# Optimization experiments

Measured on AMD Instinct MI355X. Metric: run time of the kernel, lower is better.

The kernel has to match this reference:

```python
import jax, jax.numpy as jnp
import numpy as np

B, D, K = 16384, 512, 8192
COMMITMENT_COST = 0.25


def setup_inputs() -> dict:
    key = jax.random.key(0)
    k1, k2 = jax.random.split(key)
    z = jax.random.normal(k1, (B, D), dtype=jnp.float32)
    embedding = jax.random.normal(k2, (K, D), dtype=jnp.float32)
    return {"z": z, "embedding": embedding}


def reference(z, embedding):
    # Squared L2 distances: ||z||^2 - 2 z E^T + ||e||^2  -> [B, K]
    distances = (
        jnp.sum(z * z, axis=-1, keepdims=True)
        - 2.0 * jnp.matmul(z, embedding.T)
        + jnp.sum(embedding * embedding, axis=-1)
    )
    indices = jnp.argmin(distances, axis=-1)  # [B]
    quantized = embedding[indices]  # [B, D] gather
    # use_ema=True branch: commitment loss only (codebook updated by EMA)
    commitment_loss = jnp.mean((z - jax.lax.stop_gradient(quantized)) ** 2)
    loss = COMMITMENT_COST * commitment_loss
    # Straight-through estimator
    quantized_st = z + jax.lax.stop_gradient(quantized - z)
    return quantized_st, indices, loss
```

## Files before the change

kernel.cpp:

```cpp
#include <hip/hip_runtime.h>
#include <hip/hip_bf16.h>

#define M_ROWS 16384
#define N_CODES 8192
#define DDIM    512
#define NCHUNK  512
#define MARGIN  4.0f

typedef unsigned int u32;
typedef unsigned long long u64;
typedef unsigned short u16;
typedef __attribute__((ext_vector_type(8))) short short8;
typedef __attribute__((ext_vector_type(4))) float f32x4;

__device__ __forceinline__ u32 float_to_ordered(float f) {
    u32 u = __float_as_uint(f);
    return (u & 0x80000000u) ? ~u : (u | 0x80000000u);
}

__device__ __forceinline__ u16 bf16_rne(float x) {
    u32 u = __float_as_uint(x);
    u32 r = u + 0x7FFFu + ((u >> 16) & 1u);
    return (u16)(r >> 16);
}

__device__ __forceinline__ void gl_lds16(const void* g, void* l) {
    __builtin_amdgcn_global_load_lds((const __attribute__((address_space(1))) u32*)g,
                                     (__attribute__((address_space(3))) u32*)l,
                                     16, 0, 0);
}

__device__ __forceinline__ u64 umin64(u64 a, u64 b) { return a < b ? a : b; }

#if __has_builtin(__builtin_amdgcn_update_dpp)
template <int CTRL>
__device__ __forceinline__ float dpp_mov(float x) {
    return __int_as_float(__builtin_amdgcn_update_dpp(
        __float_as_int(x), __float_as_int(x), CTRL, 0xF, 0xF, true));
}
#else
template <int CTRL>
__device__ __forceinline__ float dpp_mov(float x) {
    return __shfl_xor(x, CTRL == 0xB1 ? 1 : 2, 64);
}
#endif

__global__ __launch_bounds__(256) void vq_prep(
    const float4* __restrict__ z4, ushort4* __restrict__ zh,
    const float* __restrict__ emb, ushort4* __restrict__ eh,
    float* __restrict__ e_norms) {
    int b = blockIdx.x;
    if (b < (M_ROWS * DDIM) / 1024) {
        int i = b * 256 + threadIdx.x;
        float4 v = z4[i];
        ushort4 h;
        h.x = bf16_rne(v.x); h.y = bf16_rne(v.y);
        h.z = bf16_rne(v.z); h.w = bf16_rne(v.w);
        zh[i] = h;
    } else {
        int wave = threadIdx.x >> 6;
        int lane = threadIdx.x & 63;
        int code = (b - (M_ROWS * DDIM) / 1024) * 4 + wave;
        const float4* ep = (const float4*)(emb + (size_t)code * DDIM);
        size_t base4 = (size_t)code * (DDIM / 4);
        float s = 0.f;
        #pragma unroll
        for (int j = 0; j < 2; ++j) {
            int c = lane + 64 * j;
            float4 e = ep[c];
            s += e.x * e.x + e.y * e.y + e.z * e.z + e.w * e.w;
            ushort4 h;
            h.x = bf16_rne(e.x); h.y = bf16_rne(e.y);
            h.z = bf16_rne(e.z); h.w = bf16_rne(e.w);
            eh[base4 + c] = h;
        }
        #pragma unroll
        for (int off = 32; off; off >>= 1) s += __shfl_down(s, off, 64);
        if (lane == 0) e_norms[code] = s;
    }
}


__device__ __forceinline__ void stage_tile(const char* gbase, int kt,
                                           void* lds, int tid) {
    #pragma unroll
    for (int s = 0; s < 4; ++s) {
        const int row_l = (s << 6) + (tid >> 3);
        const int cb = (((tid & 7) ^ (row_l & 7)) << 4);
        const char* g = gbase + (size_t)row_l * (DDIM * 2) + ((size_t)kt << 7) + cb;
        char* l = (char*)lds + (s << 13) + (tid << 4);
        gl_lds16(g, l);
    }
}

#define BAR() __builtin_amdgcn_s_barrier()
#define LGK0() do { asm volatile("s_waitcnt lgkmcnt(0)" ::: "memory"); \
                    __builtin_amdgcn_sched_barrier(0); } while (0)
#define VMC8() do { asm volatile("s_waitcnt vmcnt(8)" ::: "memory"); } while (0)
#define VMC0() do { asm volatile("s_waitcnt vmcnt(0)" ::: "memory"); } while (0)

#define LDA(BUF, MH) do {                                                      \
    _Pragma("unroll") for (int i_ = 0; i_ < 4; ++i_) {                         \
        _Pragma("unroll") for (int kk_ = 0; kk_ < 2; ++kk_) {                  \
            const int row_ = (wm << 7) + ((((MH) << 2) + i_) << 4) + fr;       \
            const int cb_ = (kk_ << 6) + fkb;                                  \
            a[i_][kk_] = *(const short8*)((const char*)&ldsA[BUF][0][0]        \
                + row_ * 128 + (cb_ ^ ((row_ & 7) << 4)));                     \
        } } } while (0)

#define LDB(BUF, NH) do {                                                      \
    _Pragma("unroll") for (int j_ = 0; j_ < 2; ++j_) {                         \
        _Pragma("unroll") for (int kk_ = 0; kk_ < 2; ++kk_) {                  \
            const int row_ = (wn << 6) + ((((NH) << 1) + j_) << 4) + fr;       \
            const int cb_ = (kk_ << 6) + fkb;                                  \
            b[(NH) * 2 + j_][kk_] = *(const short8*)((const char*)&ldsB[BUF][0][0] \
                + row_ * 128 + (cb_ ^ ((row_ & 7) << 4)));                     \
        } } } while (0)

#define MFMA_Q(MH, NH) do {                                                    \
    __builtin_amdgcn_s_setprio(1);                                             \
    _Pragma("unroll") for (int i_ = 0; i_ < 4; ++i_) {                         \
        _Pragma("unroll") for (int j_ = 0; j_ < 2; ++j_) {                     \
            _Pragma("unroll") for (int kk_ = 0; kk_ < 2; ++kk_) {              \
                acc[(MH) * 4 + i_][(NH) * 2 + j_] =                            \
                    __builtin_amdgcn_mfma_f32_16x16x32_bf16(                   \
                        a[i_][kk_], b[(NH) * 2 + j_][kk_],                     \
                        acc[(MH) * 4 + i_][(NH) * 2 + j_], 0, 0, 0);           \
        } } }                                                                  \
    __builtin_amdgcn_s_setprio(0);                                             \
} while (0)

#define PH_ITER(SE, VMA, VMB, NK0, NK1)                                        \
    LDA(0, 0); LDB(0, 0);                                                      \
    BAR(); LGK0(); MFMA_Q(0, 0); BAR();                                        \
    LDB(0, 1);                                                                 \
    BAR(); LGK0(); MFMA_Q(0, 1); BAR();                                        \
    LDA(0, 1);                                                                 \
    if (SE) stage_tile(gB0, (NK0), &ldsB[0][0][0], tid);                       \
    BAR(); LGK0(); MFMA_Q(1, 0); BAR();                                        \
    if (SE) stage_tile(gA0, (NK0), &ldsA[0][0][0], tid);                       \
    BAR(); MFMA_Q(1, 1); VMA; BAR();                                           \
    LDA(1, 0); LDB(1, 0);                                                      \
    BAR(); LGK0(); MFMA_Q(0, 0); BAR();                                        \
    LDB(1, 1);                                                                 \
    BAR(); LGK0(); MFMA_Q(0, 1); BAR();                                        \
    LDA(1, 1);                                                                 \
    if (SE) stage_tile(gB0, (NK1), &ldsB[1][0][0], tid);                       \
    BAR(); LGK0(); MFMA_Q(1, 0); BAR();                                        \
    if (SE) stage_tile(gA0, (NK1), &ldsA[1][0][0], tid);                       \
    BAR(); MFMA_Q(1, 1); VMB; BAR();

__global__ __launch_bounds__(512, 2) void vq_phase1(
    const u16* __restrict__ z_hi, const u16* __restrict__ e_hi,
    const float* __restrict__ e_norms,
    float* __restrict__ chunkmin) {
    __shared__ __align__(16) u16 ldsA[2][256][64];
    __shared__ __align__(16) u16 ldsB[2][256][64];

    const int tid  = threadIdx.x;
    const int lane = tid & 63;
    const int wid  = tid >> 6;
    const int wm   = wid >> 2;
    const int wn   = wid & 3;
    const int row0 = blockIdx.x << 8;
    const int col0 = blockIdx.y << 8;
    const int fr   = lane & 15;
    const int fkb  = (lane >> 4) << 4;

    const char* gA0 = (const char*)z_hi + (size_t)row0 * (DDIM * 2);
    const char* gB0 = (const char*)e_hi + (size_t)col0 * (DDIM * 2);

    f32x4 acc[8][4] = {};
    short8 a[4][2], b[4][2];

    stage_tile(gA0, 0, &ldsA[0][0][0], tid);
    stage_tile(gB0, 0, &ldsB[0][0][0], tid);
    stage_tile(gA0, 1, &ldsA[1][0][0], tid);
    stage_tile(gB0, 1, &ldsB[1][0][0], tid);
    VMC8(); BAR();

    #pragma unroll 1
    for (int t = 0; t < 3; ++t) {
        const int nk0 = 2 * t + 2, nk1 = 2 * t + 3;
        PH_ITER(1, VMC8(), VMC8(), nk0, nk1)
    }
    PH_ITER(0, VMC0(), ((void)0), 0, 0)

    const int cn = lane & 15;
    const int cg = lane >> 4;
    float en[4];
    #pragma unroll
    for (int j = 0; j < 4; ++j) en[j] = e_norms[col0 + (wn << 6) + j * 16 + cn];

    #pragma unroll
    for (int i = 0; i < 8; ++i)
        #pragma unroll
        for (int r = 0; r < 4; ++r) {
            float mv[4];
            #pragma unroll
            for (int j = 0; j < 4; ++j) mv[j] = en[j] - 2.0f * acc[i][j][r];

            #pragma unroll
            for (int k = 0; k < 2; ++k) {
                float lo = mv[k], hi = mv[k + 2];
                float mine = (lane & 8) ? hi : lo;
                float thrs = (lane & 8) ? lo : hi;
                mv[k] = fminf(mine, __shfl_xor(thrs, 8, 64));
            }
            {
                float lo = mv[0], hi = mv[1];
                float mine = (lane & 4) ? hi : lo;
                float thrs = (lane & 4) ? lo : hi;
                mv[0] = fminf(mine, __shfl_xor(thrs, 4, 64));
            }
            mv[0] = fminf(mv[0], dpp_mov<0xB1>(mv[0]));
            mv[0] = fminf(mv[0], dpp_mov<0x4E>(mv[0]));

            if ((cn & 3) == 0) {
                const int jj = ((cn >> 3) << 1) | ((cn >> 2) & 1);
                const int row_g = row0 + (wm << 7) + (i << 4) + (cg << 2) + r;
                chunkmin[(size_t)row_g * NCHUNK + (col0 >> 4) + (wn << 2) + jj] = mv[0];
            }
        }
}

__global__ __launch_bounds__(256) void vq_finalize_rows(
    const float* __restrict__ z, const float* __restrict__ emb,
    const float* __restrict__ e_norms, const float* __restrict__ chunkmin,
    float* __restrict__ out_q, float* __restrict__ out_idx,
    float* __restrict__ partials) {
    const int wave = threadIdx.x >> 6;
    const int lane = threadIdx.x & 63;
    const int row  = blockIdx.x * 4 + wave;

    const float4* cm4 = (const float4*)(chunkmin + (size_t)row * NCHUNK);
    float4 v0 = cm4[lane];
    float4 v1 = cm4[64 + lane];
    float m = fminf(fminf(fminf(v0.x, v0.y), fminf(v0.z, v0.w)),
                    fminf(fminf(v1.x, v1.y), fminf(v1.z, v1.w)));
    #pragma unroll
    for (int off = 1; off < 64; off <<= 1) m = fminf(m, __shfl_xor(m, off, 64));
    const float thr = m + MARGIN;

    const float4* z4 = (const float4*)(z + (size_t)row * DDIM);
    float4 za = z4[2 * lane];
    float4 zb = z4[2 * lane + 1];

    u64 msk[8];
    msk[0] = __ballot(v0.x <= thr);
    msk[1] = __ballot(v0.y <= thr);
    msk[2] = __ballot(v0.z <= thr);
    msk[3] = __ballot(v0.w <= thr);
    msk[4] = __ballot(v1.x <= thr);
    msk[5] = __ballot(v1.y <= thr);
    msk[6] = __ballot(v1.z <= thr);
    msk[7] = __ballot(v1.w <= thr);

    const int cown = ((lane & 1) << 3) | ((lane & 2) << 1)
                   | ((lane & 4) >> 1) | ((lane & 8) >> 3);

    u64 best = 0xFFFFFFFFFFFFFFFFull;
    #pragma unroll
    for (int p = 0; p < 2; ++p)
        #pragma unroll
        for (int j = 0; j < 4; ++j) {
            u64 mk = msk[p * 4 + j];
            while (mk) {
                int l = __ffsll((long long)mk) - 1;
                mk &= mk - 1;
                const int chunk = (p << 8) + (l << 2) + j;
                const int cbase = chunk << 4;
                const float* eb = emb + (size_t)cbase * DDIM + lane * 8;
                float part[16];
                #pragma unroll
                for (int k = 0; k < 16; ++k) {
                    float4 ea = *(const float4*)(eb + (size_t)k * DDIM);
                    float4 e2 = *(const float4*)(eb + (size_t)k * DDIM + 4);
                    part[k] = za.x * ea.x + za.y * ea.y + za.z * ea.z + za.w * ea.w
                            + zb.x * e2.x + zb.y * e2.y + zb.z * e2.z + zb.w * e2.w;
                }
                #pragma unroll
                for (int k = 0; k < 8; ++k) {
                    float lo = part[k], hi = part[k + 8];
                    float mine = (lane & 1) ? hi : lo;
                    float thrs = (lane & 1) ? lo : hi;
                    part[k] = mine + dpp_mov<0xB1>(thrs);
                }
                #pragma unroll
                for (int k = 0; k < 4; ++k) {
                    float lo = part[k], hi = part[k + 4];
                    float mine = (lane & 2) ? hi : lo;
                    float thrs = (lane & 2) ? lo : hi;
                    part[k] = mine + dpp_mov<0x4E>(thrs);
                }
                #pragma unroll
                for (int k = 0; k < 2; ++k) {
                    float lo = part[k], hi = part[k + 2];
                    float mine = (lane & 4) ? hi : lo;
                    float thrs = (lane & 4) ? lo : hi;
                    part[k] = mine + __shfl_xor(thrs, 4, 64);
                }
                {
                    float lo = part[0], hi = part[1];
                    float mine = (lane & 8) ? hi : lo;
                    float thrs = (lane & 8) ? lo : hi;
                    part[0] = mine + __shfl_xor(thrs, 8, 64);
                }
                part[0] += __shfl_xor(part[0], 16, 64);
                part[0] += __shfl_xor(part[0], 32, 64);

                const int ci = cbase + cown;
                float dist = e_norms[ci] - 2.0f * part[0];
                best = umin64(best, ((u64)float_to_ordered(dist) << 32) | (u32)ci);
            }
        }

    #pragma unroll
    for (int off = 1; off < 64; off <<= 1)
        best = umin64(best, __shfl_xor(best, off, 64));

    const int idx = (int)(best & 0xFFFFFFFFull);
    const float* ew = emb + (size_t)idx * DDIM + lane * 8;
    float4 qa = *(const float4*)ew;
    float4 qb = *(const float4*)(ew + 4);
    float4* op = (float4*)(out_q + (size_t)row * DDIM);
    op[2 * lane]     = qa;
    op[2 * lane + 1] = qb;

    float dx, local = 0.f;
    dx = za.x - qa.x; local += dx * dx;  dx = za.y - qa.y; local += dx * dx;
    dx = za.z - qa.z; local += dx * dx;  dx = za.w - qa.w; local += dx * dx;
    dx = zb.x - qb.x; local += dx * dx;  dx = zb.y - qb.y; local += dx * dx;
    dx = zb.z - qb.z; local += dx * dx;  dx = zb.w - qb.w; local += dx * dx;
    #pragma unroll
    for (int off = 32; off; off >>= 1) local += __shfl_down(local, off, 64);

    __shared__ float wsum[4];
    if (lane == 0) { wsum[wave] = local; out_idx[row] = (float)idx; }
    __syncthreads();
    if (threadIdx.x == 0)
        partials[blockIdx.x] = wsum[0] + wsum[1] + wsum[2] + wsum[3];
}

__global__ __launch_bounds__(256) void vq_loss_reduce(
    const float* __restrict__ partials, float* __restrict__ out_loss) {
    __shared__ float red[256];
    float s = 0.f;
    for (int i = threadIdx.x; i < M_ROWS / 4; i += 256) s += partials[i];
    red[threadIdx.x] = s;
    __syncthreads();
    for (int off = 128; off; off >>= 1) {
        if (threadIdx.x < off) red[threadIdx.x] += red[threadIdx.x + off];
        __syncthreads();
    }
    if (threadIdx.x == 0)
        out_loss[0] = 0.25f * red[0] / ((float)M_ROWS * (float)DDIM);
}

extern "C" void kernel_launch(void* const* d_in, const int* in_sizes, int n_in,
                              void* d_out, int out_size, void* d_ws, size_t ws_size,
                              hipStream_t stream) {
    (void)in_sizes; (void)n_in; (void)out_size; (void)ws_size;
    const float* z   = (const float*)d_in[0];
    const float* emb = (const float*)d_in[1];

    float* out      = (float*)d_out;
    float* out_q    = out;
    float* out_idx  = out + (size_t)M_ROWS * DDIM;
    float* out_loss = out + (size_t)M_ROWS * DDIM + M_ROWS;

    char* ws = (char*)d_ws;
    float* e_norms  = (float*)ws;
    float* partials = (float*)(ws + 32768);
    u16* z_hi = (u16*)(ws + 49152);
    u16* e_hi = (u16*)(ws + 49152 + (size_t)M_ROWS * DDIM * 2);

    float* chunkmin = out_q;

    const int zblocks = (M_ROWS * DDIM) / 1024;
    const int eblocks = N_CODES / 4;
    vq_prep<<<zblocks + eblocks, 256, 0, stream>>>(
        (const float4*)z, (ushort4*)z_hi, emb, (ushort4*)e_hi, e_norms);

    vq_phase1<<<dim3(M_ROWS / 256, N_CODES / 256), 512, 0, stream>>>(
        z_hi, e_hi, e_norms, chunkmin);

    vq_finalize_rows<<<M_ROWS / 4, 256, 0, stream>>>(
        z, emb, e_norms, chunkmin, out_q, out_idx, partials);

    vq_loss_reduce<<<1, 256, 0, stream>>>(partials, out_loss);
}
```

Baseline: 356.8 us.

## Make phase1 GEMM persistent with eight row tiles per block and cross-tile prefetch

The phase-1 distance GEMM moves from a 64x32 grid of 256x256 tiles to 256 persistent blocks. Each block keeps one codebook column tile and walks 8 consecutive row tiles. The first k-slices of the next row tile are prefetched during the last k-iteration of the current one, which hides the per-tile pipeline fill and drain and keeps the codebook tile's norms in registers. In exchange, the grid of 256 blocks at two blocks per CU may leave some CUs idle or unbalanced on MI355X, and each tile's epilogue is now serialized inside the block.

```diff
diff --git a/kernel.cpp b/kernel.cpp
--- a/kernel.cpp
+++ b/kernel.cpp
@@ -98,6 +98,8 @@
                     __builtin_amdgcn_sched_barrier(0); } while (0)
 #define VMC8() do { asm volatile("s_waitcnt vmcnt(8)" ::: "memory"); } while (0)
 #define VMC0() do { asm volatile("s_waitcnt vmcnt(0)" ::: "memory"); } while (0)
+#define VMA_SEL() do { if (last) { VMC0(); } else { VMC8(); } } while (0)
+#define VMB_SEL() do { if (!last) { VMC8(); } } while (0)
 
 #define LDA(BUF, MH) do {                                                      \
     _Pragma("unroll") for (int i_ = 0; i_ < 4; ++i_) {                         \
@@ -130,24 +132,24 @@
     __builtin_amdgcn_s_setprio(0);                                             \
 } while (0)
 
-#define PH_ITER(SE, VMA, VMB, NK0, NK1)                                        \
+#define PH_ITER(SE, VMA, VMB, PA, PB, NK0, NK1)                                \
     LDA(0, 0); LDB(0, 0);                                                      \
     BAR(); LGK0(); MFMA_Q(0, 0); BAR();                                        \
     LDB(0, 1);                                                                 \
     BAR(); LGK0(); MFMA_Q(0, 1); BAR();                                        \
     LDA(0, 1);                                                                 \
-    if (SE) stage_tile(gB0, (NK0), &ldsB[0][0][0], tid);                       \
+    if (SE) stage_tile((PB), (NK0), &ldsB[0][0][0], tid);                      \
     BAR(); LGK0(); MFMA_Q(1, 0); BAR();                                        \
-    if (SE) stage_tile(gA0, (NK0), &ldsA[0][0][0], tid);                       \
+    if (SE) stage_tile((PA), (NK0), &ldsA[0][0][0], tid);                      \
     BAR(); MFMA_Q(1, 1); VMA; BAR();                                           \
     LDA(1, 0); LDB(1, 0);                                                      \
     BAR(); LGK0(); MFMA_Q(0, 0); BAR();                                        \
     LDB(1, 1);                                                                 \
     BAR(); LGK0(); MFMA_Q(0, 1); BAR();                                        \
     LDA(1, 1);                                                                 \
-    if (SE) stage_tile(gB0, (NK1), &ldsB[1][0][0], tid);                       \
+    if (SE) stage_tile((PB), (NK1), &ldsB[1][0][0], tid);                      \
     BAR(); LGK0(); MFMA_Q(1, 0); BAR();                                        \
-    if (SE) stage_tile(gA0, (NK1), &ldsA[1][0][0], tid);                       \
+    if (SE) stage_tile((PA), (NK1), &ldsA[1][0][0], tid);                      \
     BAR(); MFMA_Q(1, 1); VMB; BAR();
 
 __global__ __launch_bounds__(512, 2) void vq_phase1(
@@ -162,29 +164,18 @@
     const int wid  = tid >> 6;
     const int wm   = wid >> 2;
     const int wn   = wid & 3;
-    const int row0 = blockIdx.x << 8;
-    const int col0 = blockIdx.y << 8;
     const int fr   = lane & 15;
     const int fkb  = (lane >> 4) << 4;
 
-    const char* gA0 = (const char*)z_hi + (size_t)row0 * (DDIM * 2);
+    const int bcol  = blockIdx.x & 31;
+    const int brow0 = (blockIdx.x >> 5) << 3;
+    const int col0  = bcol << 8;
+
+    const char* gAb = (const char*)z_hi;
     const char* gB0 = (const char*)e_hi + (size_t)col0 * (DDIM * 2);
 
-    f32x4 acc[8][4] = {};
+    f32x4 acc[8][4];
     short8 a[4][2], b[4][2];
-
-    stage_tile(gA0, 0, &ldsA[0][0][0], tid);
-    stage_tile(gB0, 0, &ldsB[0][0][0], tid);
-    stage_tile(gA0, 1, &ldsA[1][0][0], tid);
-    stage_tile(gB0, 1, &ldsB[1][0][0], tid);
-    VMC8(); BAR();
-
-    #pragma unroll 1
-    for (int t = 0; t < 3; ++t) {
-        const int nk0 = 2 * t + 2, nk1 = 2 * t + 3;
-        PH_ITER(1, VMC8(), VMC8(), nk0, nk1)
-    }
-    PH_ITER(0, VMC0(), ((void)0), 0, 0)
 
     const int cn = lane & 15;
     const int cg = lane >> 4;
@@ -192,36 +183,64 @@
     #pragma unroll
     for (int j = 0; j < 4; ++j) en[j] = e_norms[col0 + (wn << 6) + j * 16 + cn];
 
-    #pragma unroll
-    for (int i = 0; i < 8; ++i)
+    {
+        const char* gA = gAb + ((size_t)brow0 << 8) * (DDIM * 2);
+        stage_tile(gA, 0, &ldsA[0][0][0], tid);
+        stage_tile(gB0, 0, &ldsB[0][0][0], tid);
+        stage_tile(gA, 1, &ldsA[1][0][0], tid);
+        stage_tile(gB0, 1, &ldsB[1][0][0], tid);
+    }
+    VMC8(); BAR();
+
+    #pragma unroll 1
+    for (int job = 0; job < 8; ++job) {
+        const int row0 = (brow0 + job) << 8;
+        const char* gAj = gAb + (size_t)row0 * (DDIM * 2);
+        const bool last = (job == 7);
+        const char* gAn = last ? gAj : (gAj + (size_t)256 * (DDIM * 2));
+
+        const f32x4 zf = {0.f, 0.f, 0.f, 0.f};
         #pragma unroll
-        for (int r = 0; r < 4; ++r) {
-            float mv[4];
+        for (int i = 0; i < 8; ++i)
             #pragma unroll
-            for (int j = 0; j < 4; ++j) mv[j] = en[j] - 2.0f * acc[i][j][r];
-
+            for (int j = 0; j < 4; ++j) acc[i][j] = zf;
+
+        PH_ITER(1, VMC8(), VMC8(), gAj, gB0, 2, 3)
+        PH_ITER(1, VMC8(), VMC8(), gAj, gB0, 4, 5)
+        PH_ITER(1, VMC8(), VMC8(), gAj, gB0, 6, 7)
+        PH_ITER(!last, VMA_SEL(), VMB_SEL(), gAn, gB0, 0, 1)
+
+        #pragma unroll
+        for (int i = 0; i < 8; ++i)
             #pragma unroll
-            for (int k = 0; k < 2; ++k) {
-                float lo = mv[k], hi = mv[k + 2];
-                float mine = (lane & 8) ? hi : lo;
-                float thrs = (lane & 8) ? lo : hi;
-                mv[k] = fminf(mine, __shfl_xor(thrs, 8, 64));
+            for (int r = 0; r < 4; ++r) {
+                float mv[4];
+                #pragma unroll
+                for (int j = 0; j < 4; ++j) mv[j] = en[j] - 2.0f * acc[i][j][r];
+
+                #pragma unroll
+                for (int k = 0; k < 2; ++k) {
+                    float lo = mv[k], hi = mv[k + 2];
+                    float mine = (lane & 8) ? hi : lo;
+                    float thrs = (lane & 8) ? lo : hi;
+                    mv[k] = fminf(mine, __shfl_xor(thrs, 8, 64));
+                }
+                {
+                    float lo = mv[0], hi = mv[1];
+                    float mine = (lane & 4) ? hi : lo;
+                    float thrs = (lane & 4) ? lo : hi;
+                    mv[0] = fminf(mine, __shfl_xor(thrs, 4, 64));
+                }
+                mv[0] = fminf(mv[0], dpp_mov<0xB1>(mv[0]));
+                mv[0] = fminf(mv[0], dpp_mov<0x4E>(mv[0]));
+
+                if ((cn & 3) == 0) {
+                    const int jj = ((cn >> 3) << 1) | ((cn >> 2) & 1);
+                    const int row_g = row0 + (wm << 7) + (i << 4) + (cg << 2) + r;
+                    chunkmin[(size_t)row_g * NCHUNK + (col0 >> 4) + (wn << 2) + jj] = mv[0];
+                }
             }
-            {
-                float lo = mv[0], hi = mv[1];
-                float mine = (lane & 4) ? hi : lo;
-                float thrs = (lane & 4) ? lo : hi;
-                mv[0] = fminf(mine, __shfl_xor(thrs, 4, 64));
-            }
-            mv[0] = fminf(mv[0], dpp_mov<0xB1>(mv[0]));
-            mv[0] = fminf(mv[0], dpp_mov<0x4E>(mv[0]));
-
-            if ((cn & 3) == 0) {
-                const int jj = ((cn >> 3) << 1) | ((cn >> 2) & 1);
-                const int row_g = row0 + (wm << 7) + (i << 4) + (cg << 2) + r;
-                chunkmin[(size_t)row_g * NCHUNK + (col0 >> 4) + (wn << 2) + jj] = mv[0];
-            }
-        }
+    }
 }
 
 __global__ __launch_bounds__(256) void vq_finalize_rows(
@@ -382,8 +401,7 @@
     vq_prep<<<zblocks + eblocks, 256, 0, stream>>>(
         (const float4*)z, (ushort4*)z_hi, emb, (ushort4*)e_hi, e_norms);
 
-    vq_phase1<<<dim3(M_ROWS / 256, N_CODES / 256), 512, 0, stream>>>(
-        z_hi, e_hi, e_norms, chunkmin);
+    vq_phase1<<<256, 512, 0, stream>>>(z_hi, e_hi, e_norms, chunkmin);
 
     vq_finalize_rows<<<M_ROWS / 4, 256, 0, stream>>>(
         z, emb, e_norms, chunkmin, out_q, out_idx, partials);
```

Measured after the change: 471.9 us. 1.32x slower.
